# Kernel tuning notes

Hardware: AMD Instinct MI355X
Metric: run time of the kernel (lower is better)

Reference implementation:

```python
import jax, jax.numpy as jnp
import numpy as np

POOL = 7
IMG = 1024.0
NUM_CLASSES = 2
R = 1000


def crop_and_resize(feat, boxes, pool):
    # feat: [C,H,W]; boxes: [N,4] normalized (y1,x1,y2,x2); returns [N,C,pool,pool]
    C, H, W = feat.shape
    y1, x1, y2, x2 = boxes[:, 0], boxes[:, 1], boxes[:, 2], boxes[:, 3]
    t = jnp.arange(pool, dtype=feat.dtype) / (pool - 1)
    ys = (y1[:, None] + (y2 - y1)[:, None] * t[None, :]) * (H - 1)  # [N,P]
    xs = (x1[:, None] + (x2 - x1)[:, None] * t[None, :]) * (W - 1)  # [N,P]
    vy = (ys >= 0) & (ys <= H - 1)
    vx = (xs >= 0) & (xs <= W - 1)
    yf = jnp.floor(ys)
    xf = jnp.floor(xs)
    wy = (ys - yf)[None, :, :, None]  # [1,N,P,1]
    wx = (xs - xf)[None, :, None, :]  # [1,N,1,P]
    y0 = jnp.clip(yf, 0, H - 1).astype(jnp.int32)
    y1i = jnp.clip(yf + 1, 0, H - 1).astype(jnp.int32)
    x0 = jnp.clip(xf, 0, W - 1).astype(jnp.int32)
    x1i = jnp.clip(xf + 1, 0, W - 1).astype(jnp.int32)

    def g(yi, xi):  # gather -> [C,N,P,P]
        return feat[:, yi[:, :, None], xi[:, None, :]]

    val = (g(y0, x0) * (1 - wy) * (1 - wx)
           + g(y0, x1i) * (1 - wy) * wx
           + g(y1i, x0) * wy * (1 - wx)
           + g(y1i, x1i) * wy * wx)
    mask = (vy[:, :, None] & vx[:, None, :])[None]  # extrapolation value 0
    return jnp.where(mask, val, 0.0).transpose(1, 0, 2, 3)


def roi_align(feats, rois_flat):
    # rois_flat: [N,4] in pixel coords (x1,y1,x2,y2)
    x1, y1, x2, y2 = rois_flat[:, 0], rois_flat[:, 1], rois_flat[:, 2], rois_flat[:, 3]
    lvl = jnp.log2(jnp.sqrt((y2 - y1) * (x2 - x1)) / 224.0)
    lvl = jnp.clip(jnp.round(lvl) + 4, 2, 5)
    boxes = rois_flat[:, jnp.array([1, 0, 3, 2])] / IMG  # (y1,x1,y2,x2) normalized
    crops = jnp.stack([crop_and_resize(f[0], boxes, POOL) for f in feats])  # [4,N,C,P,P]
    sel = (lvl[None, :] == jnp.arange(2, 6, dtype=lvl.dtype)[:, None])       # [4,N]
    return jnp.sum(jnp.where(sel[:, :, None, None, None], crops, 0.0), axis=0)  # [N,C,P,P]


def setup_inputs() -> dict:
    key = jax.random.key(0)
    ks = jax.random.split(key, 24)
    feat2 = jax.random.normal(ks[0], (1, 256, 256, 256), jnp.float32)
    feat3 = jax.random.normal(ks[1], (1, 256, 128, 128), jnp.float32)
    feat4 = jax.random.normal(ks[2], (1, 256, 64, 64), jnp.float32)
    feat5 = jax.random.normal(ks[3], (1, 256, 32, 32), jnp.float32)
    x1 = jax.random.uniform(ks[4], (1, R), minval=0.0, maxval=900.0)
    y1 = jax.random.uniform(ks[5], (1, R), minval=0.0, maxval=900.0)
    w = jax.random.uniform(ks[6], (1, R), minval=16.0, maxval=400.0)
    h = jax.random.uniform(ks[7], (1, R), minval=16.0, maxval=400.0)
    rois = jnp.stack([x1, y1, jnp.minimum(x1 + w, 1023.0), jnp.minimum(y1 + h, 1023.0)], axis=-1)
    s = 0.02
    params = dict(
        conv_w=s * jax.random.normal(ks[8], (1024, 256, POOL, POOL), jnp.float32),
        conv_b=jnp.zeros((1024,), jnp.float32),
        bn_gamma=jnp.ones((1024,), jnp.float32),
        bn_beta=jnp.zeros((1024,), jnp.float32),
        bn_mean=jnp.zeros((1024,), jnp.float32),
        bn_var=jnp.ones((1024,), jnp.float32),
        fc1_w=s * jax.random.normal(ks[9], (1024, 1024), jnp.float32),
        fc1_b=jnp.zeros((1024,), jnp.float32),
        fc2_w=s * jax.random.normal(ks[10], (1024, 1024), jnp.float32),
        fc2_b=jnp.zeros((1024,), jnp.float32),
        cls_w=s * jax.random.normal(ks[11], (NUM_CLASSES, 1024), jnp.float32),
        cls_b=jnp.zeros((NUM_CLASSES,), jnp.float32),
        bbox_w=s * jax.random.normal(ks[12], (NUM_CLASSES * 4, 1024), jnp.float32),
        bbox_b=jnp.zeros((NUM_CLASSES * 4,), jnp.float32),
    )
    return dict(feat2=feat2, feat3=feat3, feat4=feat4, feat5=feat5, rois=rois, **params)


def reference(feat2, feat3, feat4, feat5, rois, conv_w, conv_b, bn_gamma, bn_beta,
              bn_mean, bn_var, fc1_w, fc1_b, fc2_w, fc2_b, cls_w, cls_b, bbox_w, bbox_b):
    roi_number = rois.shape[1]
    pooled = roi_align([feat2, feat3, feat4, feat5], rois.reshape(-1, 4))  # [N,256,7,7]
    # conv1 (7x7 valid on 7x7 input -> 1x1 spatial) + BN (inference stats, eps=1e-3)
    y = jnp.einsum('nchw,ochw->no', pooled, conv_w) + conv_b
    y = (y - bn_mean) / jnp.sqrt(bn_var + 1e-3) * bn_gamma + bn_beta
    h = jax.nn.relu(y @ fc1_w.T + fc1_b)
    h = jax.nn.relu(h @ fc2_w.T + fc2_b)
    logits = h @ cls_w.T + cls_b
    probs = jax.nn.softmax(logits, axis=-1)
    bbox = h @ bbox_w.T + bbox_b
    return (logits.reshape(1, roi_number, NUM_CLASSES),
            probs.reshape(1, roi_number, NUM_CLASSES),
            bbox.reshape(1, roi_number, NUM_CLASSES, 4))
```

## Files before the change

kernel.cpp:

```cpp
#include <hip/hip_runtime.h>
#include <cstdint>
#include <cstddef>

typedef __attribute__((ext_vector_type(8))) short bf16x8;
typedef __attribute__((ext_vector_type(4))) float f32x4;

#define POOLK 12544
#define KPAD  12800

#define TOFF2 0
#define TOFF3 16777216
#define TOFF4 20971520
#define TOFF5 22020096

__device__ __forceinline__ void gld16(const void* g, void* l) {
    __builtin_amdgcn_global_load_lds(
        (const __attribute__((address_space(1))) void*)g,
        (__attribute__((address_space(3))) void*)l, 16, 0, 0);
}
__device__ __forceinline__ unsigned short f32_to_bf16(float f) {
    union { float f; unsigned u; } x; x.f = f;
    return (unsigned short)((x.u + 0x7FFFu + ((x.u >> 16) & 1u)) >> 16);
}
__device__ __forceinline__ float bf16_to_f32(unsigned short s) {
    return __uint_as_float(((unsigned)s) << 16);
}

__global__ __launch_bounds__(256) void feat_tr_kernel(
    const float* __restrict__ f2, const float* __restrict__ f3,
    const float* __restrict__ f4, const float* __restrict__ f5,
    unsigned short* __restrict__ T)
{
    __shared__ __align__(16) unsigned short sh[128 * 256];
    int b = blockIdx.x;
    const float* src; unsigned short* dst; int P;
    if (b < 512)      { src = f2; dst = T + TOFF2; P = 65536; }
    else if (b < 640) { src = f3; dst = T + TOFF3; P = 16384; b -= 512; }
    else if (b < 672) { src = f4; dst = T + TOFF4; P = 4096;  b -= 640; }
    else              { src = f5; dst = T + TOFF5; P = 1024;  b -= 672; }
    const int p0 = b * 128;
    const int t = threadIdx.x;
    const int lane5 = t & 31;
    const int x4 = lane5 * 4;
    const int fx = (lane5 & 7) << 3;

#pragma unroll
    for (int it = 0; it < 8; ++it) {
        float4 v[4];
        int cs[4];
#pragma unroll
        for (int u = 0; u < 4; ++u) {
            cs[u] = it * 32 + u * 8 + (t >> 5);
            v[u] = *(const float4*)(src + (size_t)cs[u] * P + p0 + x4);
        }
#pragma unroll
        for (int u = 0; u < 4; ++u) {
            const int cp = cs[u] ^ fx;
            float vv[4] = {v[u].x, v[u].y, v[u].z, v[u].w};
#pragma unroll
            for (int i = 0; i < 4; ++i)
                sh[(x4 + i) * 256 + cp] = f32_to_bf16(vv[i]);
        }
    }
    __syncthreads();

    const int c0 = lane5 * 8;
#pragma unroll
    for (int oz = 0; oz < 16; ++oz) {
        const int pp = oz * 8 + (t >> 5);
        const int cr = c0 ^ (((pp >> 2) & 7) << 3);
        const bf16x8 vv = *(const bf16x8*)&sh[pp * 256 + cr];
        *(bf16x8*)(dst + (size_t)(p0 + pp) * 256 + c0) = vv;
    }
}

__global__ __launch_bounds__(256) void gather_prep_kernel(
    const unsigned short* __restrict__ T, const float* __restrict__ rois,
    unsigned short* __restrict__ pooled, int nroi,
    const float* __restrict__ conv_w, unsigned short* __restrict__ convw_bf,
    const float* __restrict__ fc1_w, unsigned short* __restrict__ fc1w_bf,
    const float* __restrict__ fc2_w, unsigned short* __restrict__ fc2w_bf)
{
    const int t = threadIdx.x;
    const int grp = blockIdx.x / 7, rem = blockIdx.x % 7;
    const bf16x8 z8 = {};

    if (rem >= 4) {
        if (rem < 6) {
            const int o = grp * 2 + (rem - 4);
            __shared__ __align__(16) unsigned short shw[POOLK];
            const float* srow = conv_w + (size_t)o * POOLK;
            for (int k4 = t; k4 < 3136; k4 += 256) {
                const float4 v = *(const float4*)(srow + k4 * 4);
                ushort4 o4;
                o4.x = f32_to_bf16(v.x); o4.y = f32_to_bf16(v.y);
                o4.z = f32_to_bf16(v.z); o4.w = f32_to_bf16(v.w);
                *(ushort4*)(&shw[k4 * 4]) = o4;
            }
            __syncthreads();
            unsigned short* drow = convw_bf + (size_t)o * KPAD;
            for (int e = t; e < 1568; e += 256) {
                const int p = e * 8;
                const int ij = p >> 8, c0 = p & 255;
                bf16x8 o8;
#pragma unroll
                for (int c = 0; c < 8; ++c) o8[c] = (short)shw[(c0 + c) * 49 + ij];
                *(bf16x8*)(drow + p) = o8;
            }
            if (t < 32) *(bf16x8*)(drow + POOLK + t * 8) = z8;
        } else {
            const int bb = grp;
            const float* src = (bb < 256) ? fc1_w : fc2_w;
            unsigned short* dst = (bb < 256) ? fc1w_bf : fc2w_bf;
            const int base = (bb & 255) * 4096 + t * 16;
#pragma unroll
            for (int u = 0; u < 4; ++u) {
                const float4 v = *(const float4*)(src + base + u * 4);
                ushort4 o4;
                o4.x = f32_to_bf16(v.x); o4.y = f32_to_bf16(v.y);
                o4.z = f32_to_bf16(v.z); o4.w = f32_to_bf16(v.w);
                *(ushort4*)(dst + base + u * 4) = o4;
            }
        }
        return;
    }

    const int gb = grp * 4 + rem;
    const int n = gb >> 1;
    const int half = gb & 1;
    unsigned short* orow = pooled + (size_t)n * KPAD;
    if (n >= nroi) {
        const int kend = half ? KPAD : 6272;
        for (int k = half * 6272 + t * 8; k < kend; k += 2048) *(bf16x8*)(orow + k) = z8;
        return;
    }
    __shared__ int sy0[7], sy1[7], sx0[7], sx1[7];
    __shared__ float swy[7], swx[7], svy[7], svx[7];

    const float rx1 = rois[n*4+0], ry1 = rois[n*4+1];
    const float rx2 = rois[n*4+2], ry2 = rois[n*4+3];
    int lvl = (int)rintf(log2f(sqrtf((ry2-ry1)*(rx2-rx1)) * (1.0f/224.0f))) + 4;
    lvl = lvl < 2 ? 2 : (lvl > 5 ? 5 : lvl);
    const int W = 256 >> (lvl - 2);
    const float Hm1 = (float)(W - 1);
    const unsigned short* Tl = T + (lvl == 2 ? TOFF2 : (lvl == 3 ? TOFF3 : (lvl == 4 ? TOFF4 : TOFF5)));

    if (t < 7) {
        const float tt = (float)t / 6.0f;
        const float by1 = ry1*(1.0f/1024.0f), by2 = ry2*(1.0f/1024.0f);
        const float bx1 = rx1*(1.0f/1024.0f), bx2 = rx2*(1.0f/1024.0f);
        const float ys = (by1 + (by2 - by1) * tt) * Hm1;
        const float xs = (bx1 + (bx2 - bx1) * tt) * Hm1;
        const float yf = floorf(ys), xf = floorf(xs);
        swy[t] = ys - yf;  swx[t] = xs - xf;
        sy0[t] = (int)fminf(fmaxf(yf,        0.0f), Hm1);
        sy1[t] = (int)fminf(fmaxf(yf + 1.0f, 0.0f), Hm1);
        sx0[t] = (int)fminf(fmaxf(xf,        0.0f), Hm1);
        sx1[t] = (int)fminf(fmaxf(xf + 1.0f, 0.0f), Hm1);
        svy[t] = (ys >= 0.0f && ys <= Hm1) ? 1.0f : 0.0f;
        svx[t] = (xs >= 0.0f && xs <= Hm1) ? 1.0f : 0.0f;
    }
    __syncthreads();

    if (half && t < 32) *(bf16x8*)(orow + POOLK + t * 8) = z8;

    const int g    = t >> 5;
    const int c0   = (t & 31) * 8;
    const int pbeg = half * 25;
    const int pend = pbeg + 25 - half;
#pragma unroll
    for (int it = 0; it < 4; ++it) {
        const int pos = pbeg + it * 8 + g;
        if (pos >= pend) break;
        const int i = pos / 7, j = pos % 7;
        const int y0 = sy0[i], y1 = sy1[i], x0 = sx0[j], x1 = sx1[j];
        const float wy = swy[i], wx = swx[j];
        const float scale = svy[i] * svx[j];
        const bf16x8 v00 = *(const bf16x8*)(Tl + ((size_t)(y0*W + x0))*256 + c0);
        const bf16x8 v01 = *(const bf16x8*)(Tl + ((size_t)(y0*W + x1))*256 + c0);
        const bf16x8 v10 = *(const bf16x8*)(Tl + ((size_t)(y1*W + x0))*256 + c0);
        const bf16x8 v11 = *(const bf16x8*)(Tl + ((size_t)(y1*W + x1))*256 + c0);
        bf16x8 o;
#pragma unroll
        for (int jj = 0; jj < 8; ++jj) {
            const float f00 = bf16_to_f32((unsigned short)v00[jj]);
            const float f01 = bf16_to_f32((unsigned short)v01[jj]);
            const float f10 = bf16_to_f32((unsigned short)v10[jj]);
            const float f11 = bf16_to_f32((unsigned short)v11[jj]);
            const float top = f00 + (f01 - f00) * wx;
            const float bot = f10 + (f11 - f10) * wx;
            o[jj] = (short)f32_to_bf16((top + (bot - top) * wy) * scale);
        }
        *(bf16x8*)(orow + pos * 256 + c0) = o;
    }
}

__global__ __launch_bounds__(256) void roi_direct_kernel(
    const float* __restrict__ feat2, const float* __restrict__ feat3,
    const float* __restrict__ feat4, const float* __restrict__ feat5,
    const float* __restrict__ rois, unsigned short* __restrict__ pooled, int nroi)
{
    const int n = blockIdx.x;
    const int tid = threadIdx.x;
    unsigned short* orow = pooled + (size_t)n * KPAD;
    const bf16x8 z8 = {};
    if (n >= nroi) {
        for (int k = tid * 8; k < KPAD; k += 2048) *(bf16x8*)(orow + k) = z8;
        return;
    }
    if (tid < 32) *(bf16x8*)(orow + POOLK + tid * 8) = z8;
    __shared__ int sy0[7], sy1[7], sx0[7], sx1[7];
    __shared__ float swy[7], swx[7], svy[7], svx[7];
    const float rx1 = rois[n*4+0], ry1 = rois[n*4+1];
    const float rx2 = rois[n*4+2], ry2 = rois[n*4+3];
    int lvl = (int)rintf(log2f(sqrtf((ry2-ry1)*(rx2-rx1)) * (1.0f/224.0f))) + 4;
    lvl = lvl < 2 ? 2 : (lvl > 5 ? 5 : lvl);
    const int H = 256 >> (lvl - 2);
    const float Hm1 = (float)(H - 1);
    const float* feat = lvl==2 ? feat2 : (lvl==3 ? feat3 : (lvl==4 ? feat4 : feat5));
    if (tid < 7) {
        const float t = (float)tid / 6.0f;
        const float by1 = ry1*(1.0f/1024.0f), by2 = ry2*(1.0f/1024.0f);
        const float bx1 = rx1*(1.0f/1024.0f), bx2 = rx2*(1.0f/1024.0f);
        const float ys = (by1 + (by2-by1)*t) * Hm1;
        const float xs = (bx1 + (bx2-bx1)*t) * Hm1;
        const float yf = floorf(ys), xf = floorf(xs);
        swy[tid] = ys - yf;  swx[tid] = xs - xf;
        sy0[tid] = (int)fminf(fmaxf(yf,      0.0f), Hm1);
        sy1[tid] = (int)fminf(fmaxf(yf+1.0f, 0.0f), Hm1);
        sx0[tid] = (int)fminf(fmaxf(xf,      0.0f), Hm1);
        sx1[tid] = (int)fminf(fmaxf(xf+1.0f, 0.0f), Hm1);
        svy[tid] = (ys >= 0.0f && ys <= Hm1) ? 1.0f : 0.0f;
        svx[tid] = (xs >= 0.0f && xs <= Hm1) ? 1.0f : 0.0f;
    }
    __syncthreads();
    const int HW = H * H;
    for (int e = tid; e < POOLK; e += 256) {
        const int c = e / 49, ij = e % 49, i = ij / 7, j = ij % 7;
        const float* p = feat + c * HW;
        const int y0 = sy0[i], y1 = sy1[i], x0 = sx0[j], x1 = sx1[j];
        const float wy = swy[i], wx = swx[j];
        const float v00 = p[y0*H + x0], v01 = p[y0*H + x1];
        const float v10 = p[y1*H + x0], v11 = p[y1*H + x1];
        float v = v00*(1.0f-wy)*(1.0f-wx) + v01*(1.0f-wy)*wx
                + v10*wy*(1.0f-wx)        + v11*wy*wx;
        v *= svy[i] * svx[j];
        orow[ij*256 + c] = f32_to_bf16(v);
    }
}

__global__ __launch_bounds__(256) void wprep_kernel(
    const float* __restrict__ conv_w, unsigned short* __restrict__ convw_bf,
    const float* __restrict__ fc1_w, unsigned short* __restrict__ fc1w_bf,
    const float* __restrict__ fc2_w, unsigned short* __restrict__ fc2w_bf)
{
    const int t = threadIdx.x;
    int b = blockIdx.x;
    if (b < 1024) {
        __shared__ __align__(16) unsigned short shw[POOLK];
        const float* srow = conv_w + (size_t)b * POOLK;
        for (int k4 = t; k4 < 3136; k4 += 256) {
            const float4 v = *(const float4*)(srow + k4 * 4);
            ushort4 o4;
            o4.x = f32_to_bf16(v.x); o4.y = f32_to_bf16(v.y);
            o4.z = f32_to_bf16(v.z); o4.w = f32_to_bf16(v.w);
            *(ushort4*)(&shw[k4 * 4]) = o4;
        }
        __syncthreads();
        unsigned short* drow = convw_bf + (size_t)b * KPAD;
        for (int e = t; e < 1568; e += 256) {
            const int p = e * 8;
            const int ij = p >> 8, c0 = p & 255;
            bf16x8 o8;
#pragma unroll
            for (int c = 0; c < 8; ++c) o8[c] = (short)shw[(c0 + c) * 49 + ij];
            *(bf16x8*)(drow + p) = o8;
        }
        const bf16x8 z8 = {};
        if (t < 32) *(bf16x8*)(drow + POOLK + t * 8) = z8;
        return;
    }
    b -= 1024;
    const float* src = (b < 256) ? fc1_w : fc2_w;
    unsigned short* dst = (b < 256) ? fc1w_bf : fc2w_bf;
    const int base = (b & 255) * 4096 + t * 16;
#pragma unroll
    for (int u = 0; u < 4; ++u) {
        const float4 v = *(const float4*)(src + base + u * 4);
        ushort4 o4;
        o4.x = f32_to_bf16(v.x); o4.y = f32_to_bf16(v.y);
        o4.z = f32_to_bf16(v.z); o4.w = f32_to_bf16(v.w);
        *(ushort4*)(dst + base + u * 4) = o4;
    }
}

__global__ __launch_bounds__(256, 4) void gemm_bt(
    const unsigned short* __restrict__ A, const unsigned short* __restrict__ B,
    unsigned short* __restrict__ Cpart, int K, int Kper, int nz)
{
    __shared__ __align__(16) unsigned short At[128 * 32];
    __shared__ __align__(16) unsigned short Bt[128 * 32];
    const int tid  = threadIdx.x;
    const int lane = tid & 63;
    const int bid  = blockIdx.x;
    int z, iq;
    if (nz == 16) { z = (bid & 7) * 2 + ((bid >> 3) & 1); iq = bid >> 4; }
    else          { z = bid % nz;                          iq = bid / nz; }
    const int bx = iq & 7, by = iq >> 3;
    const int wm = (tid >> 6) >> 1, wn = (tid >> 6) & 1;
    const size_t k0 = (size_t)z * Kper;

    const int r1 = tid >> 2;
    const int csw = (((tid & 3) ^ ((tid >> 3) & 3))) * 8;
    const unsigned short* Ag = A + ((size_t)(by * 128 + r1)) * K + k0 + csw;
    const unsigned short* Bg = B + ((size_t)(bx * 128 + r1)) * K + k0 + csw;
    const int nit = Kper >> 5;

    f32x4 acc[4][4] = {};
    const int fr = lane & 15;
    const int fq = lane >> 4;
    const int sx = (fr >> 1) & 3;

    for (int it = 0; it < nit; ++it) {
        const size_t ko = (size_t)it * 32;
        gld16(Ag + ko,                  &At[tid * 8]);
        gld16(Ag + (size_t)64 * K + ko, &At[(tid + 256) * 8]);
        gld16(Bg + ko,                  &Bt[tid * 8]);
        gld16(Bg + (size_t)64 * K + ko, &Bt[(tid + 256) * 8]);
        asm volatile("s_waitcnt vmcnt(0)" ::: "memory");
        __syncthreads();

        bf16x8 a[4], b[4];
#pragma unroll
        for (int mi = 0; mi < 4; ++mi) {
            const int m = wm * 64 + mi * 16 + fr;
            a[mi] = *(const bf16x8*)&At[m * 32 + ((fq ^ sx) << 3)];
        }
#pragma unroll
        for (int ni = 0; ni < 4; ++ni) {
            const int m = wn * 64 + ni * 16 + fr;
            b[ni] = *(const bf16x8*)&Bt[m * 32 + ((fq ^ sx) << 3)];
        }
#pragma unroll
        for (int mi = 0; mi < 4; ++mi)
#pragma unroll
            for (int ni = 0; ni < 4; ++ni)
                acc[mi][ni] = __builtin_amdgcn_mfma_f32_16x16x32_bf16(
                    a[mi], b[ni], acc[mi][ni], 0, 0, 0);
        __syncthreads();
    }

    unsigned short* Cp = Cpart + (size_t)z * (1024 * 1024);
    const int row0 = by * 128 + wm * 64;
    const int col0 = bx * 128 + wn * 64;
#pragma unroll
    for (int mi = 0; mi < 4; ++mi)
#pragma unroll
        for (int ni = 0; ni < 4; ++ni)
#pragma unroll
            for (int r = 0; r < 4; ++r)
                Cp[(size_t)(row0 + mi*16 + fq*4 + r) * 1024 + col0 + ni*16 + fr]
                    = f32_to_bf16(acc[mi][ni][r]);
}

__global__ void reduce_bn_kernel(const unsigned short* __restrict__ part,
    const float* __restrict__ bias, const float* __restrict__ gamma,
    const float* __restrict__ beta, const float* __restrict__ mean,
    const float* __restrict__ var, unsigned short* __restrict__ out, int nz)
{
    const int i4 = (blockIdx.x * 256 + threadIdx.x) * 4;
    const int n = i4 & 1023;
    float4 v = make_float4(0.f, 0.f, 0.f, 0.f);
    for (int zz = 0; zz < nz; ++zz) {
        const ushort4 p = *(const ushort4*)(part + (size_t)zz * 1048576 + i4);
        v.x += bf16_to_f32(p.x); v.y += bf16_to_f32(p.y);
        v.z += bf16_to_f32(p.z); v.w += bf16_to_f32(p.w);
    }
    const float4 bi = *(const float4*)(bias + n);
    const float4 ga = *(const float4*)(gamma + n);
    const float4 be = *(const float4*)(beta + n);
    const float4 me = *(const float4*)(mean + n);
    const float4 va = *(const float4*)(var + n);
    ushort4 o;
    o.x = f32_to_bf16((v.x + bi.x - me.x) * __frsqrt_rn(va.x + 0.001f) * ga.x + be.x);
    o.y = f32_to_bf16((v.y + bi.y - me.y) * __frsqrt_rn(va.y + 0.001f) * ga.y + be.y);
    o.z = f32_to_bf16((v.z + bi.z - me.z) * __frsqrt_rn(va.z + 0.001f) * ga.z + be.z);
    o.w = f32_to_bf16((v.w + bi.w - me.w) * __frsqrt_rn(va.w + 0.001f) * ga.w + be.w);
    *(ushort4*)(out + i4) = o;
}

__global__ __launch_bounds__(256) void gemm64_fused(
    const unsigned short* __restrict__ A, const unsigned short* __restrict__ B,
    const float* __restrict__ bias, unsigned short* __restrict__ out, int relu)
{
    __shared__ __align__(16) unsigned short At[2][64*64];
    __shared__ __align__(16) unsigned short Bt[2][64*64];
    const int tid = threadIdx.x, lane = tid & 63;
    const int w = tid >> 6, wm = w >> 1, wn = w & 1;
    const int r1 = tid >> 3;
    const int q  = tid & 7;
    const int csw = (q ^ (r1 & 7)) * 8;
    const unsigned short* Ag = A + (size_t)(blockIdx.y*64 + r1) * 1024 + csw;
    const unsigned short* Bg = B + (size_t)(blockIdx.x*64 + r1) * 1024 + csw;
    const int fr = lane & 15, fq = lane >> 4;
    const int sA = fr & 7;

#pragma unroll
    for (int p = 0; p < 2; ++p) {
        gld16(Ag + (size_t)(32 * p) * 1024, &At[0][p * 2048 + tid * 8]);
        gld16(Bg + (size_t)(32 * p) * 1024, &Bt[0][p * 2048 + tid * 8]);
    }

    f32x4 acc[2][2] = {};
    int buf = 0;
    for (int it = 0; it < 16; ++it) {
        if (it + 1 < 16) {
            const int ko = (it + 1) * 64;
#pragma unroll
            for (int p = 0; p < 2; ++p) {
                gld16(Ag + (size_t)(32 * p) * 1024 + ko, &At[buf ^ 1][p * 2048 + tid * 8]);
                gld16(Bg + (size_t)(32 * p) * 1024 + ko, &Bt[buf ^ 1][p * 2048 + tid * 8]);
            }
            asm volatile("s_waitcnt vmcnt(4)" ::: "memory");
        } else {
            asm volatile("s_waitcnt vmcnt(0)" ::: "memory");
        }
        __builtin_amdgcn_sched_barrier(0);
        __builtin_amdgcn_s_barrier();
        __builtin_amdgcn_sched_barrier(0);

        bf16x8 a[2][2], b[2][2];
#pragma unroll
        for (int mi = 0; mi < 2; ++mi) {
            const int row = wm * 32 + mi * 16 + fr;
#pragma unroll
            for (int kk = 0; kk < 2; ++kk)
                a[mi][kk] = *(const bf16x8*)&At[buf][row * 64 + ((kk * 4 + fq) ^ sA) * 8];
        }
#pragma unroll
        for (int ni = 0; ni < 2; ++ni) {
            const int row = wn * 32 + ni * 16 + fr;
#pragma unroll
            for (int kk = 0; kk < 2; ++kk)
                b[ni][kk] = *(const bf16x8*)&Bt[buf][row * 64 + ((kk * 4 + fq) ^ sA) * 8];
        }
        __builtin_amdgcn_s_setprio(1);
#pragma unroll
        for (int kk = 0; kk < 2; ++kk)
#pragma unroll
            for (int mi = 0; mi < 2; ++mi)
#pragma unroll
                for (int ni = 0; ni < 2; ++ni)
                    acc[mi][ni] = __builtin_amdgcn_mfma_f32_16x16x32_bf16(
                        a[mi][kk], b[ni][kk], acc[mi][ni], 0, 0, 0);
        __builtin_amdgcn_s_setprio(0);
        __builtin_amdgcn_sched_barrier(0);
        __builtin_amdgcn_s_barrier();
        __builtin_amdgcn_sched_barrier(0);
        buf ^= 1;
    }
    const int row0 = blockIdx.y*64 + wm*32;
    const int col0 = blockIdx.x*64 + wn*32;
#pragma unroll
    for (int mi = 0; mi < 2; ++mi)
#pragma unroll
        for (int ni = 0; ni < 2; ++ni)
#pragma unroll
            for (int r = 0; r < 4; ++r) {
                const int row = row0 + mi*16 + fq*4 + r;
                const int col = col0 + ni*16 + fr;
                float v = acc[mi][ni][r] + bias[col];
                if (relu) v = fmaxf(v, 0.0f);
                out[(size_t)row * 1024 + col] = f32_to_bf16(v);
            }
}

__global__ __launch_bounds__(256) void head_kernel(
    const unsigned short* __restrict__ h2,
    const float* __restrict__ cls_w, const float* __restrict__ cls_b,
    const float* __restrict__ bbox_w, const float* __restrict__ bbox_b,
    float* __restrict__ out)
{
    const int roi = blockIdx.x * 4 + (threadIdx.x >> 6);
    const int lane = threadIdx.x & 63;
    const unsigned short* hrow = h2 + (size_t)roi * 1024;
    float hv[16];
#pragma unroll
    for (int j = 0; j < 16; ++j)
        hv[j] = bf16_to_f32(hrow[lane*16 + j]);
    float r[10];
#pragma unroll
    for (int o = 0; o < 10; ++o) {
        const float* w = (o < 2) ? (cls_w + o*1024) : (bbox_w + (size_t)(o-2)*1024);
        float s = 0.f;
#pragma unroll
        for (int j = 0; j < 16; ++j) s += hv[j] * w[lane*16 + j];
#pragma unroll
        for (int off = 32; off > 0; off >>= 1) s += __shfl_xor(s, off);
        r[o] = s;
    }
    if (lane == 0) {
        const float l0 = r[0] + cls_b[0], l1 = r[1] + cls_b[1];
        out[roi*2+0] = l0; out[roi*2+1] = l1;
        const float m = fmaxf(l0, l1);
        const float e0 = expf(l0 - m), e1 = expf(l1 - m);
        const float inv = 1.0f / (e0 + e1);
        out[2000 + roi*2 + 0] = e0 * inv;
        out[2000 + roi*2 + 1] = e1 * inv;
#pragma unroll
        for (int qq = 0; qq < 8; ++qq) out[4000 + roi*8 + qq] = r[2+qq] + bbox_b[qq];
    }
}

extern "C" void kernel_launch(void* const* d_in, const int* in_sizes, int n_in,
                              void* d_out, int out_size, void* d_ws, size_t ws_size,
                              hipStream_t stream)
{
    const float* feat2   = (const float*)d_in[0];
    const float* feat3   = (const float*)d_in[1];
    const float* feat4   = (const float*)d_in[2];
    const float* feat5   = (const float*)d_in[3];
    const float* rois    = (const float*)d_in[4];
    const float* conv_w  = (const float*)d_in[5];
    const float* conv_b  = (const float*)d_in[6];
    const float* bn_gamma= (const float*)d_in[7];
    const float* bn_beta = (const float*)d_in[8];
    const float* bn_mean = (const float*)d_in[9];
    const float* bn_var  = (const float*)d_in[10];
    const float* fc1_w   = (const float*)d_in[11];
    const float* fc1_b   = (const float*)d_in[12];
    const float* fc2_w   = (const float*)d_in[13];
    const float* fc2_b   = (const float*)d_in[14];
    const float* cls_w   = (const float*)d_in[15];
    const float* cls_b   = (const float*)d_in[16];
    const float* bbox_w  = (const float*)d_in[17];
    const float* bbox_b  = (const float*)d_in[18];
    float* out = (float*)d_out;
    const int nroi = in_sizes[4] / 4;

    const size_t poolBytes = (size_t)1024 * KPAD * 2;
    const size_t fixedBytes = 2 * poolBytes + 5 * (size_t)2097152;
    const size_t needA = fixedBytes + (size_t)44564480;
    const int tier = (ws_size >= needA) ? 1 : 2;
    const size_t regionA = tier == 1 ? (size_t)44564480 : (size_t)16777216;
    const int nzc  = tier == 1 ? 16 : 8;
    const int Kper = tier == 1 ? 800 : 1600;

    char* ws = (char*)d_ws;
    size_t off = 0;
    auto alloc = [&](size_t bytes) {
        void* p = ws + off; off += (bytes + 255) & ~(size_t)255; return p;
    };
    char* rA = (char*)alloc(regionA);
    unsigned short* T    = (unsigned short*)rA;
    unsigned short* part = (unsigned short*)rA;
    unsigned short* pooled   = (unsigned short*)alloc(poolBytes);
    unsigned short* convw_bf = (unsigned short*)alloc(poolBytes);
    unsigned short* fc1w_bf  = (unsigned short*)alloc((size_t)1048576 * 2);
    unsigned short* fc2w_bf  = (unsigned short*)alloc((size_t)1048576 * 2);
    unsigned short* ybf      = (unsigned short*)alloc((size_t)1048576 * 2);
    unsigned short* h1bf     = (unsigned short*)alloc((size_t)1048576 * 2);
    unsigned short* h2bf     = (unsigned short*)alloc((size_t)1048576 * 2);

    if (tier == 1) {
        hipLaunchKernelGGL(feat_tr_kernel, dim3(680), dim3(256), 0, stream,
                           feat2, feat3, feat4, feat5, T);
        hipLaunchKernelGGL(gather_prep_kernel, dim3(3584), dim3(256), 0, stream,
                           T, rois, pooled, nroi,
                           conv_w, convw_bf, fc1_w, fc1w_bf, fc2_w, fc2w_bf);
    } else {
        hipLaunchKernelGGL(wprep_kernel, dim3(1536), dim3(256), 0, stream,
                           conv_w, convw_bf, fc1_w, fc1w_bf, fc2_w, fc2w_bf);
        hipLaunchKernelGGL(roi_direct_kernel, dim3(1024), dim3(256), 0, stream,
                           feat2, feat3, feat4, feat5, rois, pooled, nroi);
    }

    hipLaunchKernelGGL(gemm_bt, dim3(64 * nzc), dim3(256), 0, stream,
                       pooled, convw_bf, part, KPAD, Kper, nzc);
    hipLaunchKernelGGL(reduce_bn_kernel, dim3(1024), dim3(256), 0, stream,
                       part, conv_b, bn_gamma, bn_beta, bn_mean, bn_var, ybf, nzc);

    hipLaunchKernelGGL(gemm64_fused, dim3(16, 16), dim3(256), 0, stream,
                       ybf, fc1w_bf, fc1_b, h1bf, 1);
    hipLaunchKernelGGL(gemm64_fused, dim3(16, 16), dim3(256), 0, stream,
                       h1bf, fc2w_bf, fc2_b, h2bf, 1);

    hipLaunchKernelGGL(head_kernel, dim3(250), dim3(256), 0, stream,
                       h2bf, cls_w, cls_b, bbox_w, bbox_b, out);
}
```

Before: 125.8 us.

## Overlap level-2 feature transpose with weight prep and non-level-2 ROI gathers

The large level-2 feature transpose moves out of the standalone transpose kernel into the merged prep kernel, where it runs alongside the weight conversion and the gathers for ROIs on levels 3-5. ROIs on level 2 are deferred to a new gather2 kernel launched afterward. The goal is to overlap the big transpose with independent work instead of serialising it before every gather. The cost is an extra kernel launch and a larger merged grid with a 32KB shared buffer per block, which may lower occupancy for the gather blocks.

After: 131.2 us. 1.04x slower.

```diff
diff --git a/kernel.cpp b/kernel.cpp
--- a/kernel.cpp
+++ b/kernel.cpp
@@ -25,19 +25,23 @@
 __device__ __forceinline__ float bf16_to_f32(unsigned short s) {
     return __uint_as_float(((unsigned)s) << 16);
 }
-
-__global__ __launch_bounds__(256) void feat_tr_kernel(
-    const float* __restrict__ f2, const float* __restrict__ f3,
-    const float* __restrict__ f4, const float* __restrict__ f5,
-    unsigned short* __restrict__ T)
+__device__ __forceinline__ int roi_level(const float* rois, int n) {
+    const float rx1 = rois[n*4+0], ry1 = rois[n*4+1];
+    const float rx2 = rois[n*4+2], ry2 = rois[n*4+3];
+    int lvl = (int)rintf(log2f(sqrtf((ry2-ry1)*(rx2-rx1)) * (1.0f/224.0f))) + 4;
+    return lvl < 2 ? 2 : (lvl > 5 ? 5 : lvl);
+}
+
+__global__ __launch_bounds__(256) void feat_tr345_kernel(
+    const float* __restrict__ f3, const float* __restrict__ f4,
+    const float* __restrict__ f5, unsigned short* __restrict__ T)
 {
     __shared__ __align__(16) unsigned short sh[128 * 256];
     int b = blockIdx.x;
     const float* src; unsigned short* dst; int P;
-    if (b < 512)      { src = f2; dst = T + TOFF2; P = 65536; }
-    else if (b < 640) { src = f3; dst = T + TOFF3; P = 16384; b -= 512; }
-    else if (b < 672) { src = f4; dst = T + TOFF4; P = 4096;  b -= 640; }
-    else              { src = f5; dst = T + TOFF5; P = 1024;  b -= 672; }
+    if (b < 128)      { src = f3; dst = T + TOFF3; P = 16384; }
+    else if (b < 160) { src = f4; dst = T + TOFF4; P = 4096;  b -= 128; }
+    else              { src = f5; dst = T + TOFF5; P = 1024;  b -= 160; }
     const int p0 = b * 128;
     const int t = threadIdx.x;
     const int lane5 = t & 31;
@@ -74,28 +78,54 @@
     }
 }
 
-__global__ __launch_bounds__(256) void gather_prep_kernel(
-    const unsigned short* __restrict__ T, const float* __restrict__ rois,
-    unsigned short* __restrict__ pooled, int nroi,
+__global__ __launch_bounds__(256) void merged_prep_kernel(
+    const float* __restrict__ f2, unsigned short* __restrict__ T,
+    const float* __restrict__ rois, unsigned short* __restrict__ pooled, int nroi,
     const float* __restrict__ conv_w, unsigned short* __restrict__ convw_bf,
     const float* __restrict__ fc1_w, unsigned short* __restrict__ fc1w_bf,
     const float* __restrict__ fc2_w, unsigned short* __restrict__ fc2w_bf)
 {
+    __shared__ __align__(16) unsigned short shbuf[16384];
     const int t = threadIdx.x;
-    const int grp = blockIdx.x / 7, rem = blockIdx.x % 7;
+    const int grp = blockIdx.x / 9, rem = blockIdx.x % 9;
     const bf16x8 z8 = {};
 
-    if (rem >= 4) {
-        if (rem < 6) {
-            const int o = grp * 2 + (rem - 4);
-            __shared__ __align__(16) unsigned short shw[POOLK];
+    if (rem < 2) {
+        const int tile = grp * 2 + rem;
+        const int p0 = tile * 64;
+        const int pr = t & 15;
+        const int ch = t >> 4;
+        const int key = (pr & 7) << 3;
+#pragma unroll
+        for (int cc = 0; cc < 16; ++cc) {
+            const int c = cc * 16 + ch;
+            const float4 v = *(const float4*)(f2 + (size_t)c * 65536 + p0 + pr * 4);
+            float vv[4] = {v.x, v.y, v.z, v.w};
+#pragma unroll
+            for (int i = 0; i < 4; ++i)
+                shbuf[(pr * 4 + i) * 256 + (c ^ key)] = f32_to_bf16(vv[i]);
+        }
+        __syncthreads();
+#pragma unroll
+        for (int pass = 0; pass < 8; ++pass) {
+            const int chunk = pass * 256 + t;
+            const int pp = chunk >> 5, c0 = (chunk & 31) * 8;
+            const int rkey = ((pp >> 2) & 7) << 3;
+            const bf16x8 vv = *(const bf16x8*)&shbuf[pp * 256 + (c0 ^ rkey)];
+            *(bf16x8*)(T + TOFF2 + (size_t)(p0 + pp) * 256 + c0) = vv;
+        }
+        return;
+    }
+    if (rem >= 6) {
+        if (rem < 8) {
+            const int o = grp * 2 + (rem - 6);
             const float* srow = conv_w + (size_t)o * POOLK;
             for (int k4 = t; k4 < 3136; k4 += 256) {
                 const float4 v = *(const float4*)(srow + k4 * 4);
                 ushort4 o4;
                 o4.x = f32_to_bf16(v.x); o4.y = f32_to_bf16(v.y);
                 o4.z = f32_to_bf16(v.z); o4.w = f32_to_bf16(v.w);
-                *(ushort4*)(&shw[k4 * 4]) = o4;
+                *(ushort4*)(&shbuf[k4 * 4]) = o4;
             }
             __syncthreads();
             unsigned short* drow = convw_bf + (size_t)o * KPAD;
@@ -104,7 +134,7 @@
                 const int ij = p >> 8, c0 = p & 255;
                 bf16x8 o8;
 #pragma unroll
-                for (int c = 0; c < 8; ++c) o8[c] = (short)shw[(c0 + c) * 49 + ij];
+                for (int c = 0; c < 8; ++c) o8[c] = (short)shbuf[(c0 + c) * 49 + ij];
                 *(bf16x8*)(drow + p) = o8;
             }
             if (t < 32) *(bf16x8*)(drow + POOLK + t * 8) = z8;
@@ -125,7 +155,7 @@
         return;
     }
 
-    const int gb = grp * 4 + rem;
+    const int gb = grp * 4 + (rem - 2);
     const int n = gb >> 1;
     const int half = gb & 1;
     unsigned short* orow = pooled + (size_t)n * KPAD;
@@ -134,19 +164,19 @@
         for (int k = half * 6272 + t * 8; k < kend; k += 2048) *(bf16x8*)(orow + k) = z8;
         return;
     }
+    if (half && t < 32) *(bf16x8*)(orow + POOLK + t * 8) = z8;
+    const int lvl = roi_level(rois, n);
+    if (lvl == 2) return;
+
+    const int W = 256 >> (lvl - 2);
+    const float Hm1 = (float)(W - 1);
+    const unsigned short* Tl = T + (lvl == 3 ? TOFF3 : (lvl == 4 ? TOFF4 : TOFF5));
     __shared__ int sy0[7], sy1[7], sx0[7], sx1[7];
     __shared__ float swy[7], swx[7], svy[7], svx[7];
-
-    const float rx1 = rois[n*4+0], ry1 = rois[n*4+1];
-    const float rx2 = rois[n*4+2], ry2 = rois[n*4+3];
-    int lvl = (int)rintf(log2f(sqrtf((ry2-ry1)*(rx2-rx1)) * (1.0f/224.0f))) + 4;
-    lvl = lvl < 2 ? 2 : (lvl > 5 ? 5 : lvl);
-    const int W = 256 >> (lvl - 2);
-    const float Hm1 = (float)(W - 1);
-    const unsigned short* Tl = T + (lvl == 2 ? TOFF2 : (lvl == 3 ? TOFF3 : (lvl == 4 ? TOFF4 : TOFF5)));
-
     if (t < 7) {
         const float tt = (float)t / 6.0f;
+        const float ry1 = rois[n*4+1], ry2 = rois[n*4+3];
+        const float rx1 = rois[n*4+0], rx2 = rois[n*4+2];
         const float by1 = ry1*(1.0f/1024.0f), by2 = ry2*(1.0f/1024.0f);
         const float bx1 = rx1*(1.0f/1024.0f), bx2 = rx2*(1.0f/1024.0f);
         const float ys = (by1 + (by2 - by1) * tt) * Hm1;
@@ -162,8 +192,6 @@
     }
     __syncthreads();
 
-    if (half && t < 32) *(bf16x8*)(orow + POOLK + t * 8) = z8;
-
     const int g    = t >> 5;
     const int c0   = (t & 31) * 8;
     const int pbeg = half * 25;
@@ -195,6 +223,72 @@
     }
 }
 
+__global__ __launch_bounds__(256) void gather2_kernel(
+    const unsigned short* __restrict__ T, const float* __restrict__ rois,
+    unsigned short* __restrict__ pooled, int nroi)
+{
+    const int t = threadIdx.x;
+    const int gb = blockIdx.x;
+    const int n = gb >> 1;
+    const int half = gb & 1;
+    if (n >= nroi) return;
+    if (roi_level(rois, n) != 2) return;
+    unsigned short* orow = pooled + (size_t)n * KPAD;
+    const int W = 256;
+    const float Hm1 = 255.0f;
+    const unsigned short* Tl = T + TOFF2;
+    __shared__ int sy0[7], sy1[7], sx0[7], sx1[7];
+    __shared__ float swy[7], swx[7], svy[7], svx[7];
+    if (t < 7) {
+        const float tt = (float)t / 6.0f;
+        const float ry1 = rois[n*4+1], ry2 = rois[n*4+3];
+        const float rx1 = rois[n*4+0], rx2 = rois[n*4+2];
+        const float by1 = ry1*(1.0f/1024.0f), by2 = ry2*(1.0f/1024.0f);
+        const float bx1 = rx1*(1.0f/1024.0f), bx2 = rx2*(1.0f/1024.0f);
+        const float ys = (by1 + (by2 - by1) * tt) * Hm1;
+        const float xs = (bx1 + (bx2 - bx1) * tt) * Hm1;
+        const float yf = floorf(ys), xf = floorf(xs);
+        swy[t] = ys - yf;  swx[t] = xs - xf;
+        sy0[t] = (int)fminf(fmaxf(yf,        0.0f), Hm1);
+        sy1[t] = (int)fminf(fmaxf(yf + 1.0f, 0.0f), Hm1);
+        sx0[t] = (int)fminf(fmaxf(xf,        0.0f), Hm1);
+        sx1[t] = (int)fminf(fmaxf(xf + 1.0f, 0.0f), Hm1);
+        svy[t] = (ys >= 0.0f && ys <= Hm1) ? 1.0f : 0.0f;
+        svx[t] = (xs >= 0.0f && xs <= Hm1) ? 1.0f : 0.0f;
+    }
+    __syncthreads();
+
+    const int g    = t >> 5;
+    const int c0   = (t & 31) * 8;
+    const int pbeg = half * 25;
+    const int pend = pbeg + 25 - half;
+#pragma unroll
+    for (int it = 0; it < 4; ++it) {
+        const int pos = pbeg + it * 8 + g;
+        if (pos >= pend) break;
+        const int i = pos / 7, j = pos % 7;
+        const int y0 = sy0[i], y1 = sy1[i], x0 = sx0[j], x1 = sx1[j];
+        const float wy = swy[i], wx = swx[j];
+        const float scale = svy[i] * svx[j];
+        const bf16x8 v00 = *(const bf16x8*)(Tl + ((size_t)(y0*W + x0))*256 + c0);
+        const bf16x8 v01 = *(const bf16x8*)(Tl + ((size_t)(y0*W + x1))*256 + c0);
+        const bf16x8 v10 = *(const bf16x8*)(Tl + ((size_t)(y1*W + x0))*256 + c0);
+        const bf16x8 v11 = *(const bf16x8*)(Tl + ((size_t)(y1*W + x1))*256 + c0);
+        bf16x8 o;
+#pragma unroll
+        for (int jj = 0; jj < 8; ++jj) {
+            const float f00 = bf16_to_f32((unsigned short)v00[jj]);
+            const float f01 = bf16_to_f32((unsigned short)v01[jj]);
+            const float f10 = bf16_to_f32((unsigned short)v10[jj]);
+            const float f11 = bf16_to_f32((unsigned short)v11[jj]);
+            const float top = f00 + (f01 - f00) * wx;
+            const float bot = f10 + (f11 - f10) * wx;
+            o[jj] = (short)f32_to_bf16((top + (bot - top) * wy) * scale);
+        }
+        *(bf16x8*)(orow + pos * 256 + c0) = o;
+    }
+}
+
 __global__ __launch_bounds__(256) void roi_direct_kernel(
     const float* __restrict__ feat2, const float* __restrict__ feat3,
     const float* __restrict__ feat4, const float* __restrict__ feat5,
@@ -211,15 +305,14 @@
     if (tid < 32) *(bf16x8*)(orow + POOLK + tid * 8) = z8;
     __shared__ int sy0[7], sy1[7], sx0[7], sx1[7];
     __shared__ float swy[7], swx[7], svy[7], svx[7];
-    const float rx1 = rois[n*4+0], ry1 = rois[n*4+1];
-    const float rx2 = rois[n*4+2], ry2 = rois[n*4+3];
-    int lvl = (int)rintf(log2f(sqrtf((ry2-ry1)*(rx2-rx1)) * (1.0f/224.0f))) + 4;
-    lvl = lvl < 2 ? 2 : (lvl > 5 ? 5 : lvl);
+    const int lvl = roi_level(rois, n);
     const int H = 256 >> (lvl - 2);
     const float Hm1 = (float)(H - 1);
     const float* feat = lvl==2 ? feat2 : (lvl==3 ? feat3 : (lvl==4 ? feat4 : feat5));
     if (tid < 7) {
         const float t = (float)tid / 6.0f;
+        const float ry1 = rois[n*4+1], ry2 = rois[n*4+3];
+        const float rx1 = rois[n*4+0], rx2 = rois[n*4+2];
         const float by1 = ry1*(1.0f/1024.0f), by2 = ry2*(1.0f/1024.0f);
         const float bx1 = rx1*(1.0f/1024.0f), bx2 = rx2*(1.0f/1024.0f);
         const float ys = (by1 + (by2-by1)*t) * Hm1;
@@ -563,11 +656,13 @@
     unsigned short* h2bf     = (unsigned short*)alloc((size_t)1048576 * 2);
 
     if (tier == 1) {
-        hipLaunchKernelGGL(feat_tr_kernel, dim3(680), dim3(256), 0, stream,
-                           feat2, feat3, feat4, feat5, T);
-        hipLaunchKernelGGL(gather_prep_kernel, dim3(3584), dim3(256), 0, stream,
-                           T, rois, pooled, nroi,
+        hipLaunchKernelGGL(feat_tr345_kernel, dim3(168), dim3(256), 0, stream,
+                           feat3, feat4, feat5, T);
+        hipLaunchKernelGGL(merged_prep_kernel, dim3(4608), dim3(256), 0, stream,
+                           feat2, T, rois, pooled, nroi,
                            conv_w, convw_bf, fc1_w, fc1w_bf, fc2_w, fc2w_bf);
+        hipLaunchKernelGGL(gather2_kernel, dim3(2048), dim3(256), 0, stream,
+                           T, rois, pooled, nroi);
     } else {
         hipLaunchKernelGGL(wprep_kernel, dim3(1536), dim3(256), 0, stream,
                            conv_w, convw_bf, fc1_w, fc1w_bf, fc2_w, fc2w_bf);
```
